# Performance work log

Measured on AMD Instinct MI355X. Metric: run time of the kernel, lower is better.

## Reference

```python
import jax, jax.numpy as jnp
import numpy as np

B, L, D, H, E = 8, 256, 128, 6, 32

def setup_inputs() -> dict:
    key = jax.random.key(0)
    ks = jax.random.split(key, 9)
    s = 0.02
    return {
        "x": jax.random.normal(ks[0], (B, L, D), jnp.float32),
        "weight_adj": jax.random.uniform(ks[1], (B, H, L, L), jnp.float32),
        "e": jax.random.normal(ks[2], (B, L, L, E), jnp.float32),
        "W_w": jax.random.normal(ks[3], (D, D), jnp.float32) * s,
        "W_b": jax.random.normal(ks[4], (D,), jnp.float32) * s,
        "Wx_w": jax.random.normal(ks[5], (H, H + 2 * D + E), jnp.float32) * s,
        "Wx_b": jax.random.normal(ks[6], (H,), jnp.float32) * s,
        "Wxx_w": jax.random.normal(ks[7], (D, D), jnp.float32) * s,
        "Wxx_b": jax.random.normal(ks[8], (D,), jnp.float32) * s,
    }

def reference(x, weight_adj, e, W_w, W_b, Wx_w, Wx_b, Wxx_w, Wxx_b):
    d = x.shape[-1]
    h = weight_adj.shape[1]
    # mean over heads, then graph conv + linear + relu
    adj_avg = weight_adj.mean(axis=1)                      # [B,L,L]
    gcn = jax.nn.relu(jnp.einsum('bij,bjd->bid', adj_avg, x) @ W_w.T + W_b)  # [B,L,d]
    # Wx applied to cat([weight_adj_perm, node_i, node_j, e], -1), decomposed
    # column-wise so the huge [B,L,L,2d+H+E] concat is never materialized;
    # math is identical to Linear(cat(...)).
    Wa  = Wx_w[:, :h]                 # [H,H]
    Wn1 = Wx_w[:, h:h + d]            # [H,d]
    Wn2 = Wx_w[:, h + d:h + 2 * d]    # [H,d]
    We  = Wx_w[:, h + 2 * d:]         # [H,E]
    adj_term = jnp.einsum('bhij,kh->bijk', weight_adj, Wa)   # [B,L,L,H]
    n1 = gcn @ Wn1.T                                          # [B,L,H] (row node)
    n2 = gcn @ Wn2.T                                          # [B,L,H] (col node)
    e_term = jnp.einsum('bije,ke->bijk', e, We)               # [B,L,L,H]
    new_adj = adj_term + n1[:, :, None, :] + n2[:, None, :, :] + e_term + Wx_b
    new_adj = jnp.transpose(new_adj, (0, 3, 1, 2))            # [B,H,L,L]
    out = gcn @ Wxx_w.T + Wxx_b                               # [B,L,d]
    return out, new_adj
```

## Files before the change

### kernel.cpp

```cpp
#include <hip/hip_runtime.h>

#define Bn 8
#define Ln 256
#define Dn 128
#define Hn 6
#define En 32
#define WXROW (Hn + 2*Dn + En)
#define ROWS 4

__global__ __launch_bounds__(256) void k_gcn(
    const float* __restrict__ x, const float* __restrict__ wadj,
    const float* __restrict__ W_w, const float* __restrict__ W_b,
    const float* __restrict__ Wx_w,
    const float* __restrict__ Wxx_w, const float* __restrict__ Wxx_b,
    float* __restrict__ out, float* __restrict__ n1_ws, float* __restrict__ n2_ws)
{
    __shared__ float adj[ROWS][Ln];
    __shared__ float part[8][ROWS][Dn];
    __shared__ float t_s[ROWS][Dn];
    __shared__ float g_s[ROWS][Dn];

    const int t  = threadIdx.x;
    const int b  = blockIdx.x >> 6;
    const int i0 = (blockIdx.x & 63) * ROWS;

    {
        const int r  = t >> 6;
        const int j4 = t & 63;
        const float4* w4 = (const float4*)wadj;
        float4 sum = {0.f, 0.f, 0.f, 0.f};
        #pragma unroll
        for (int h = 0; h < Hn; ++h) {
            const float4 v = w4[(((size_t)b * Hn + h) * Ln + (i0 + r)) * (Ln / 4) + j4];
            sum.x += v.x; sum.y += v.y; sum.z += v.z; sum.w += v.w;
        }
        const float inv_h = 1.0f / 6.0f;
        sum.x *= inv_h; sum.y *= inv_h; sum.z *= inv_h; sum.w *= inv_h;
        ((float4*)&adj[0][0])[r * (Ln / 4) + j4] = sum;
    }
    __syncthreads();

    {
        const int q  = t >> 5;
        const int d4 = t & 31;
        float4 acc[ROWS];
        #pragma unroll
        for (int r = 0; r < ROWS; ++r) acc[r] = {0.f, 0.f, 0.f, 0.f};

        const float4* xp4 = (const float4*)(x + (size_t)b * Ln * Dn) + d4;
        const float4* adj4 = (const float4*)&adj[0][0];
        const int j0 = q * 32;

        #pragma unroll 2
        for (int jj4 = 0; jj4 < 8; ++jj4) {
            const int j = j0 + jj4 * 4;
            const float4 xv0 = xp4[(size_t)(j + 0) * 32];
            const float4 xv1 = xp4[(size_t)(j + 1) * 32];
            const float4 xv2 = xp4[(size_t)(j + 2) * 32];
            const float4 xv3 = xp4[(size_t)(j + 3) * 32];
            #pragma unroll
            for (int r = 0; r < ROWS; ++r) {
                const float4 a = adj4[r * (Ln / 4) + (j >> 2)];
                float4 v = acc[r];
                v.x = fmaf(a.x, xv0.x, v.x); v.y = fmaf(a.x, xv0.y, v.y);
                v.z = fmaf(a.x, xv0.z, v.z); v.w = fmaf(a.x, xv0.w, v.w);
                v.x = fmaf(a.y, xv1.x, v.x); v.y = fmaf(a.y, xv1.y, v.y);
                v.z = fmaf(a.y, xv1.z, v.z); v.w = fmaf(a.y, xv1.w, v.w);
                v.x = fmaf(a.z, xv2.x, v.x); v.y = fmaf(a.z, xv2.y, v.y);
                v.z = fmaf(a.z, xv2.z, v.z); v.w = fmaf(a.z, xv2.w, v.w);
                v.x = fmaf(a.w, xv3.x, v.x); v.y = fmaf(a.w, xv3.y, v.y);
                v.z = fmaf(a.w, xv3.z, v.z); v.w = fmaf(a.w, xv3.w, v.w);
                acc[r] = v;
            }
        }
        #pragma unroll
        for (int r = 0; r < ROWS; ++r)
            ((float4*)&part[q][r][0])[d4] = acc[r];
    }
    __syncthreads();

    {
        const int d  = t & 127;
        const int rr = t >> 7;
        #pragma unroll
        for (int rq = 0; rq < 2; ++rq) {
            const int r = rr + rq * 2;
            float s = 0.f;
            #pragma unroll
            for (int q = 0; q < 8; ++q) s += part[q][r][d];
            t_s[r][d] = s;
        }
    }
    __syncthreads();

    {
        const int s = t >> 7, d = t & 127;
        const int r0 = s, r1 = s + 2;
        float a0 = W_b[d], a1 = a0;
        const float4* wr = (const float4*)(W_w + (size_t)d * Dn);
        const float4* t0 = (const float4*)&t_s[r0][0];
        const float4* t1 = (const float4*)&t_s[r1][0];
        #pragma unroll 8
        for (int c4 = 0; c4 < Dn / 4; ++c4) {
            const float4 w = wr[c4];
            const float4 u0 = t0[c4];
            const float4 u1 = t1[c4];
            a0 = fmaf(u0.x, w.x, a0); a0 = fmaf(u0.y, w.y, a0);
            a0 = fmaf(u0.z, w.z, a0); a0 = fmaf(u0.w, w.w, a0);
            a1 = fmaf(u1.x, w.x, a1); a1 = fmaf(u1.y, w.y, a1);
            a1 = fmaf(u1.z, w.z, a1); a1 = fmaf(u1.w, w.w, a1);
        }
        g_s[r0][d] = fmaxf(a0, 0.f);
        g_s[r1][d] = fmaxf(a1, 0.f);
    }
    __syncthreads();

    {
        const int s = t >> 7, d = t & 127;
        const int r0 = s, r1 = s + 2;
        float a0 = Wxx_b[d], a1 = a0;
        const float4* wr = (const float4*)(Wxx_w + (size_t)d * Dn);
        const float4* g0 = (const float4*)&g_s[r0][0];
        const float4* g1 = (const float4*)&g_s[r1][0];
        #pragma unroll 8
        for (int c4 = 0; c4 < Dn / 4; ++c4) {
            const float4 w = wr[c4];
            const float4 u0 = g0[c4];
            const float4 u1 = g1[c4];
            a0 = fmaf(u0.x, w.x, a0); a0 = fmaf(u0.y, w.y, a0);
            a0 = fmaf(u0.z, w.z, a0); a0 = fmaf(u0.w, w.w, a0);
            a1 = fmaf(u1.x, w.x, a1); a1 = fmaf(u1.y, w.y, a1);
            a1 = fmaf(u1.z, w.z, a1); a1 = fmaf(u1.w, w.w, a1);
        }
        out[((size_t)b * Ln + (i0 + r0)) * Dn + d] = a0;
        out[((size_t)b * Ln + (i0 + r1)) * Dn + d] = a1;
    }

    if (t < ROWS * 2 * Hn) {
        const int r  = t / (2 * Hn);
        const int kk = t % (2 * Hn);
        const int k  = (kk < Hn) ? kk : (kk - Hn);
        const bool isn2 = (kk >= Hn);
        const float* wrow = Wx_w + (size_t)k * WXROW + Hn + (isn2 ? Dn : 0);
        float acc = 0.f;
        #pragma unroll 8
        for (int c = 0; c < Dn; ++c)
            acc = fmaf(g_s[r][c], wrow[c], acc);
        const size_t idx = ((size_t)b * Hn + k) * Ln + (i0 + r);
        if (isn2) n2_ws[idx] = acc;
        else      n1_ws[idx] = acc;
    }
}

#define EPAD 33
__global__ __launch_bounds__(256) void k_adj(
    const float* __restrict__ wadj, const float* __restrict__ e,
    const float* __restrict__ Wx_w, const float* __restrict__ Wx_b,
    const float* __restrict__ n1_ws, const float* __restrict__ n2_ws,
    float* __restrict__ new_adj)
{
    __shared__ float e_lds[Ln * EPAD];
    __shared__ float Wa_s[Hn][Hn];
    __shared__ float We_s[Hn][En];
    __shared__ float bias_n1[Hn];

    const int t = threadIdx.x;
    const int b = blockIdx.x >> 8;
    const int i = blockIdx.x & 255;

    if (t < Hn * Hn) {
        const int k = t / Hn, h = t % Hn;
        Wa_s[k][h] = Wx_w[(size_t)k * WXROW + h];
    }
    if (t >= 64 && t < 64 + Hn * En) {
        const int q = t - 64, k = q / En, c = q % En;
        We_s[k][c] = Wx_w[(size_t)k * WXROW + Hn + 2 * Dn + c];
    }
    if (t >= 32 && t < 32 + Hn) {
        const int k = t - 32;
        bias_n1[k] = Wx_b[k] + n1_ws[((size_t)b * Hn + k) * Ln + i];
    }

    {
        const float4* ep4 = (const float4*)(e + (((size_t)b * Ln + i) * Ln) * En);
        #pragma unroll
        for (int k = 0; k < 8; ++k) {
            const int idx = t + k * 256;
            const float4 v = ep4[idx];
            const int j = idx >> 3;
            const int c = (idx & 7) * 4;
            float* dst = &e_lds[j * EPAD + c];
            dst[0] = v.x; dst[1] = v.y; dst[2] = v.z; dst[3] = v.w;
        }
    }
    __syncthreads();

    const int j = t;

    float ev[En];
    {
        const float* src = &e_lds[j * EPAD];
        #pragma unroll
        for (int c = 0; c < En; ++c) ev[c] = src[c];
    }

    float wv[Hn];
    #pragma unroll
    for (int h = 0; h < Hn; ++h)
        wv[h] = wadj[(((size_t)b * Hn + h) * Ln + i) * Ln + j];

    float n2v[Hn];
    #pragma unroll
    for (int k = 0; k < Hn; ++k)
        n2v[k] = n2_ws[((size_t)b * Hn + k) * Ln + j];

    #pragma unroll
    for (int k = 0; k < Hn; ++k) {
        float acc = bias_n1[k] + n2v[k];
        #pragma unroll
        for (int h = 0; h < Hn; ++h)
            acc = fmaf(wv[h], Wa_s[k][h], acc);
        #pragma unroll
        for (int c = 0; c < En; ++c)
            acc = fmaf(ev[c], We_s[k][c], acc);
        new_adj[(((size_t)b * Hn + k) * Ln + i) * Ln + j] = acc;
    }
}

extern "C" void kernel_launch(void* const* d_in, const int* in_sizes, int n_in,
                              void* d_out, int out_size, void* d_ws, size_t ws_size,
                              hipStream_t stream) {
    const float* x      = (const float*)d_in[0];
    const float* wadj   = (const float*)d_in[1];
    const float* e      = (const float*)d_in[2];
    const float* W_w    = (const float*)d_in[3];
    const float* W_b    = (const float*)d_in[4];
    const float* Wx_w   = (const float*)d_in[5];
    const float* Wx_b   = (const float*)d_in[6];
    const float* Wxx_w  = (const float*)d_in[7];
    const float* Wxx_b  = (const float*)d_in[8];

    float* out      = (float*)d_out;
    float* new_adj  = out + (size_t)Bn * Ln * Dn;

    float* n1_ws = (float*)d_ws;
    float* n2_ws = n1_ws + (size_t)Bn * Hn * Ln;

    k_gcn<<<Bn * (Ln / ROWS), 256, 0, stream>>>(x, wadj, W_w, W_b, Wx_w,
                                                Wxx_w, Wxx_b, out, n1_ws, n2_ws);
    k_adj<<<Bn * Ln, 256, 0, stream>>>(wadj, e, Wx_w, Wx_b, n1_ws, n2_ws, new_adj);
}
```

Before: 146.0 us.

## Split head-averaging kernel, widen GCN blocks, chunk edge-feature staging in adj kernel

The head-mean of weight_adj moves into its own kernel that writes to workspace. The GCN kernel now uses 512 threads and splits the neighbour sum and both 128x128 linears across thread groups, with reductions through shared memory. The adj kernel stages the edge features for 128 columns at a time, which halves its LDS footprint to raise occupancy, and each thread half computes 3 of the 6 output heads. The costs are an extra launch, an avg buffer in workspace, and redundant weight_adj loads across the two thread halves.

```diff
diff --git a/kernel.cpp b/kernel.cpp
--- a/kernel.cpp
+++ b/kernel.cpp
@@ -8,15 +8,34 @@
 #define WXROW (Hn + 2*Dn + En)
 #define ROWS 4
 
-__global__ __launch_bounds__(256) void k_gcn(
-    const float* __restrict__ x, const float* __restrict__ wadj,
+__global__ __launch_bounds__(256) void k_avg(
+    const float* __restrict__ wadj, float* __restrict__ avg)
+{
+    const int g = blockIdx.x * 256 + threadIdx.x;
+    const int j4 = g & 63;
+    const int i  = (g >> 6) & 255;
+    const int b  = g >> 14;
+    const float4* w4 = (const float4*)wadj;
+    float4 s = {0.f, 0.f, 0.f, 0.f};
+    #pragma unroll
+    for (int h = 0; h < Hn; ++h) {
+        const float4 v = w4[(((size_t)b * Hn + h) * Ln + i) * (Ln / 4) + j4];
+        s.x += v.x; s.y += v.y; s.z += v.z; s.w += v.w;
+    }
+    const float inv_h = 1.0f / 6.0f;
+    s.x *= inv_h; s.y *= inv_h; s.z *= inv_h; s.w *= inv_h;
+    ((float4*)avg)[g] = s;
+}
+
+__global__ __launch_bounds__(512) void k_gcn2(
+    const float* __restrict__ x, const float* __restrict__ avg,
     const float* __restrict__ W_w, const float* __restrict__ W_b,
     const float* __restrict__ Wx_w,
     const float* __restrict__ Wxx_w, const float* __restrict__ Wxx_b,
     float* __restrict__ out, float* __restrict__ n1_ws, float* __restrict__ n2_ws)
 {
     __shared__ float adj[ROWS][Ln];
-    __shared__ float part[8][ROWS][Dn];
+    __shared__ float part[16][ROWS][Dn];
     __shared__ float t_s[ROWS][Dn];
     __shared__ float g_s[ROWS][Dn];
 
@@ -24,20 +43,8 @@
     const int b  = blockIdx.x >> 6;
     const int i0 = (blockIdx.x & 63) * ROWS;
 
-    {
-        const int r  = t >> 6;
-        const int j4 = t & 63;
-        const float4* w4 = (const float4*)wadj;
-        float4 sum = {0.f, 0.f, 0.f, 0.f};
-        #pragma unroll
-        for (int h = 0; h < Hn; ++h) {
-            const float4 v = w4[(((size_t)b * Hn + h) * Ln + (i0 + r)) * (Ln / 4) + j4];
-            sum.x += v.x; sum.y += v.y; sum.z += v.z; sum.w += v.w;
-        }
-        const float inv_h = 1.0f / 6.0f;
-        sum.x *= inv_h; sum.y *= inv_h; sum.z *= inv_h; sum.w *= inv_h;
-        ((float4*)&adj[0][0])[r * (Ln / 4) + j4] = sum;
-    }
+    if (t < 256)
+        ((float4*)&adj[0][0])[t] = ((const float4*)avg)[((size_t)b << 14) + (i0 << 6) + t];
     __syncthreads();
 
     {
@@ -46,21 +53,18 @@
         float4 acc[ROWS];
         #pragma unroll
         for (int r = 0; r < ROWS; ++r) acc[r] = {0.f, 0.f, 0.f, 0.f};
-
-        const float4* xp4 = (const float4*)(x + (size_t)b * Ln * Dn) + d4;
+        const float4* xp4  = (const float4*)(x + (size_t)b * Ln * Dn) + d4;
         const float4* adj4 = (const float4*)&adj[0][0];
-        const int j0 = q * 32;
-
-        #pragma unroll 2
-        for (int jj4 = 0; jj4 < 8; ++jj4) {
-            const int j = j0 + jj4 * 4;
+        #pragma unroll
+        for (int jj4 = 0; jj4 < 4; ++jj4) {
+            const int j = q * 16 + jj4 * 4;
             const float4 xv0 = xp4[(size_t)(j + 0) * 32];
             const float4 xv1 = xp4[(size_t)(j + 1) * 32];
             const float4 xv2 = xp4[(size_t)(j + 2) * 32];
             const float4 xv3 = xp4[(size_t)(j + 3) * 32];
             #pragma unroll
             for (int r = 0; r < ROWS; ++r) {
-                const float4 a = adj4[r * (Ln / 4) + (j >> 2)];
+                const float4 a = adj4[r * 64 + (j >> 2)];
                 float4 v = acc[r];
                 v.x = fmaf(a.x, xv0.x, v.x); v.y = fmaf(a.x, xv0.y, v.y);
                 v.z = fmaf(a.x, xv0.z, v.z); v.w = fmaf(a.x, xv0.w, v.w);
@@ -80,60 +84,70 @@
     __syncthreads();
 
     {
-        const int d  = t & 127;
-        const int rr = t >> 7;
-        #pragma unroll
-        for (int rq = 0; rq < 2; ++rq) {
-            const int r = rr + rq * 2;
-            float s = 0.f;
-            #pragma unroll
-            for (int q = 0; q < 8; ++q) s += part[q][r][d];
-            t_s[r][d] = s;
-        }
-    }
-    __syncthreads();
-
-    {
-        const int s = t >> 7, d = t & 127;
-        const int r0 = s, r1 = s + 2;
-        float a0 = W_b[d], a1 = a0;
-        const float4* wr = (const float4*)(W_w + (size_t)d * Dn);
-        const float4* t0 = (const float4*)&t_s[r0][0];
-        const float4* t1 = (const float4*)&t_s[r1][0];
-        #pragma unroll 8
-        for (int c4 = 0; c4 < Dn / 4; ++c4) {
+        const int rr = t >> 7, d = t & 127;
+        float s = 0.f;
+        #pragma unroll
+        for (int q = 0; q < 16; ++q) s += part[q][rr][d];
+        t_s[rr][d] = s;
+    }
+    __syncthreads();
+
+    {
+        const int s = t >> 7, d = t & 127, c0 = s * 32;
+        const float4* wr = (const float4*)(W_w + (size_t)d * Dn + c0);
+        float acc[ROWS] = {0.f, 0.f, 0.f, 0.f};
+        #pragma unroll
+        for (int c4 = 0; c4 < 8; ++c4) {
             const float4 w = wr[c4];
-            const float4 u0 = t0[c4];
-            const float4 u1 = t1[c4];
-            a0 = fmaf(u0.x, w.x, a0); a0 = fmaf(u0.y, w.y, a0);
-            a0 = fmaf(u0.z, w.z, a0); a0 = fmaf(u0.w, w.w, a0);
-            a1 = fmaf(u1.x, w.x, a1); a1 = fmaf(u1.y, w.y, a1);
-            a1 = fmaf(u1.z, w.z, a1); a1 = fmaf(u1.w, w.w, a1);
-        }
-        g_s[r0][d] = fmaxf(a0, 0.f);
-        g_s[r1][d] = fmaxf(a1, 0.f);
-    }
-    __syncthreads();
-
-    {
-        const int s = t >> 7, d = t & 127;
-        const int r0 = s, r1 = s + 2;
-        float a0 = Wxx_b[d], a1 = a0;
-        const float4* wr = (const float4*)(Wxx_w + (size_t)d * Dn);
-        const float4* g0 = (const float4*)&g_s[r0][0];
-        const float4* g1 = (const float4*)&g_s[r1][0];
-        #pragma unroll 8
-        for (int c4 = 0; c4 < Dn / 4; ++c4) {
+            #pragma unroll
+            for (int r = 0; r < ROWS; ++r) {
+                const float4 u = ((const float4*)&t_s[r][c0])[c4];
+                float a = acc[r];
+                a = fmaf(u.x, w.x, a); a = fmaf(u.y, w.y, a);
+                a = fmaf(u.z, w.z, a); a = fmaf(u.w, w.w, a);
+                acc[r] = a;
+            }
+        }
+        #pragma unroll
+        for (int r = 0; r < ROWS; ++r) part[s][r][d] = acc[r];
+    }
+    __syncthreads();
+
+    {
+        const int rr = t >> 7, d = t & 127;
+        const float v = part[0][rr][d] + part[1][rr][d] + part[2][rr][d]
+                      + part[3][rr][d] + W_b[d];
+        g_s[rr][d] = fmaxf(v, 0.f);
+    }
+    __syncthreads();
+
+    {
+        const int s = t >> 7, d = t & 127, c0 = s * 32;
+        const float4* wr = (const float4*)(Wxx_w + (size_t)d * Dn + c0);
+        float acc[ROWS] = {0.f, 0.f, 0.f, 0.f};
+        #pragma unroll
+        for (int c4 = 0; c4 < 8; ++c4) {
             const float4 w = wr[c4];
-            const float4 u0 = g0[c4];
-            const float4 u1 = g1[c4];
-            a0 = fmaf(u0.x, w.x, a0); a0 = fmaf(u0.y, w.y, a0);
-            a0 = fmaf(u0.z, w.z, a0); a0 = fmaf(u0.w, w.w, a0);
-            a1 = fmaf(u1.x, w.x, a1); a1 = fmaf(u1.y, w.y, a1);
-            a1 = fmaf(u1.z, w.z, a1); a1 = fmaf(u1.w, w.w, a1);
-        }
-        out[((size_t)b * Ln + (i0 + r0)) * Dn + d] = a0;
-        out[((size_t)b * Ln + (i0 + r1)) * Dn + d] = a1;
+            #pragma unroll
+            for (int r = 0; r < ROWS; ++r) {
+                const float4 u = ((const float4*)&g_s[r][c0])[c4];
+                float a = acc[r];
+                a = fmaf(u.x, w.x, a); a = fmaf(u.y, w.y, a);
+                a = fmaf(u.z, w.z, a); a = fmaf(u.w, w.w, a);
+                acc[r] = a;
+            }
+        }
+        __syncthreads();
+        #pragma unroll
+        for (int r = 0; r < ROWS; ++r) part[s][r][t & 127] = acc[r];
+    }
+    __syncthreads();
+
+    {
+        const int rr = t >> 7, d = t & 127;
+        const float v = part[0][rr][d] + part[1][rr][d] + part[2][rr][d]
+                      + part[3][rr][d] + Wxx_b[d];
+        out[((size_t)b * Ln + (i0 + rr)) * Dn + d] = v;
     }
 
     if (t < ROWS * 2 * Hn) {
@@ -159,7 +173,7 @@
     const float* __restrict__ n1_ws, const float* __restrict__ n2_ws,
     float* __restrict__ new_adj)
 {
-    __shared__ float e_lds[Ln * EPAD];
+    __shared__ float e_lds[128 * EPAD];
     __shared__ float Wa_s[Hn][Hn];
     __shared__ float We_s[Hn][En];
     __shared__ float bias_n1[Hn];
@@ -181,49 +195,45 @@
         bias_n1[k] = Wx_b[k] + n1_ws[((size_t)b * Hn + k) * Ln + i];
     }
 
-    {
-        const float4* ep4 = (const float4*)(e + (((size_t)b * Ln + i) * Ln) * En);
-        #pragma unroll
-        for (int k = 0; k < 8; ++k) {
-            const int idx = t + k * 256;
-            const float4 v = ep4[idx];
+    const float4* ep4 = (const float4*)(e + (((size_t)b * Ln + i) * Ln) * En);
+    const int s  = t >> 7;
+    const int jl = t & 127;
+
+    #pragma unroll
+    for (int cH = 0; cH < 2; ++cH) {
+        __syncthreads();
+        #pragma unroll
+        for (int p = 0; p < 4; ++p) {
+            const int idx = t + p * 256;
+            const float4 v = ep4[cH * 1024 + idx];
             const int j = idx >> 3;
             const int c = (idx & 7) * 4;
             float* dst = &e_lds[j * EPAD + c];
             dst[0] = v.x; dst[1] = v.y; dst[2] = v.z; dst[3] = v.w;
         }
-    }
-    __syncthreads();
-
-    const int j = t;
-
-    float ev[En];
-    {
-        const float* src = &e_lds[j * EPAD];
-        #pragma unroll
-        for (int c = 0; c < En; ++c) ev[c] = src[c];
-    }
-
-    float wv[Hn];
-    #pragma unroll
-    for (int h = 0; h < Hn; ++h)
-        wv[h] = wadj[(((size_t)b * Hn + h) * Ln + i) * Ln + j];
-
-    float n2v[Hn];
-    #pragma unroll
-    for (int k = 0; k < Hn; ++k)
-        n2v[k] = n2_ws[((size_t)b * Hn + k) * Ln + j];
-
-    #pragma unroll
-    for (int k = 0; k < Hn; ++k) {
-        float acc = bias_n1[k] + n2v[k];
+        __syncthreads();
+
+        const int j = cH * 128 + jl;
+
+        float wv[Hn];
         #pragma unroll
         for (int h = 0; h < Hn; ++h)
-            acc = fmaf(wv[h], Wa_s[k][h], acc);
-        #pragma unroll
-        for (int c = 0; c < En; ++c)
-            acc = fmaf(ev[c], We_s[k][c], acc);
-        new_adj[(((size_t)b * Hn + k) * Ln + i) * Ln + j] = acc;
+            wv[h] = wadj[(((size_t)b * Hn + h) * Ln + i) * Ln + j];
+
+        const float* ev = &e_lds[jl * EPAD];
+
+        #pragma unroll
+        for (int kq = 0; kq < 3; ++kq) {
+            const int k = s * 3 + kq;
+            float acc = bias_n1[k] + n2_ws[((size_t)b * Hn + k) * Ln + j];
+            #pragma unroll
+            for (int h = 0; h < Hn; ++h)
+                acc = fmaf(wv[h], Wa_s[k][h], acc);
+            #pragma unroll
+            for (int c = 0; c < En; ++c)
+                acc = fmaf(ev[c], We_s[k][c], acc);
+            new_adj[(((size_t)b * Hn + k) * Ln + i) * Ln + j] = acc;
+        }
     }
 }
 
@@ -245,8 +255,10 @@
 
     float* n1_ws = (float*)d_ws;
     float* n2_ws = n1_ws + (size_t)Bn * Hn * Ln;
-
-    k_gcn<<<Bn * (Ln / ROWS), 256, 0, stream>>>(x, wadj, W_w, W_b, Wx_w,
-                                                Wxx_w, Wxx_b, out, n1_ws, n2_ws);
+    float* avg   = n2_ws + (size_t)Bn * Hn * Ln;
+
+    k_avg<<<(Bn * Ln * Ln / 4) / 256, 256, 0, stream>>>(wadj, avg);
+    k_gcn2<<<Bn * (Ln / ROWS), 512, 0, stream>>>(x, avg, W_w, W_b, Wx_w,
+                                                 Wxx_w, Wxx_b, out, n1_ws, n2_ws);
     k_adj<<<Bn * Ln, 256, 0, stream>>>(wadj, e, Wx_w, Wx_b, n1_ws, n2_ws, new_adj);
 }
```

New measurement: 150.0 us. 1.03x slower.

## Split adjacency-times-x into tiled split-K kernel with LDS-staged x

Applied to the files above, without the earlier changes.

The head-mean adjacency product with x moves out of the fused gcn kernel into its own kernel. That kernel tiles 32 rows by 64 columns, stages x in shared memory so it is reused across 32 rows, and writes four split-K partials to workspace. A second kernel sums the partials and runs the two linear layers and the n1/n2 projections as before. The aim is to stop every 4-row block from rereading the whole of x from global memory. The cost is an extra launch plus a workspace write and read of four full partial tensors.

```diff
diff --git a/kernel.cpp b/kernel.cpp
--- a/kernel.cpp
+++ b/kernel.cpp
@@ -6,90 +6,96 @@
 #define Hn 6
 #define En 32
 #define WXROW (Hn + 2*Dn + En)
-#define ROWS 4
-
-__global__ __launch_bounds__(256) void k_gcn(
-    const float* __restrict__ x, const float* __restrict__ wadj,
+
+__global__ __launch_bounds__(512) void kT(
+    const float* __restrict__ wadj, const float* __restrict__ x,
+    float* __restrict__ T)
+{
+    __shared__ float adj_s[32][68];
+    __shared__ float x_s[32][128];
+
+    const int t   = threadIdx.x;
+    const int blk = blockIdx.x;
+    const int jq  = blk & 3;
+    const int it  = (blk >> 2) & 7;
+    const int b   = blk >> 5;
+    const int i0  = it * 32;
+
+    {
+        const int row = t >> 4, j4 = t & 15;
+        const float4* w4 = (const float4*)wadj;
+        float4 s = {0.f, 0.f, 0.f, 0.f};
+        #pragma unroll
+        for (int h = 0; h < Hn; ++h) {
+            const float4 v = w4[(((size_t)b * Hn + h) * Ln + i0 + row) * 64 + jq * 16 + j4];
+            s.x += v.x; s.y += v.y; s.z += v.z; s.w += v.w;
+        }
+        const float inv_h = 1.0f / 6.0f;
+        s.x *= inv_h; s.y *= inv_h; s.z *= inv_h; s.w *= inv_h;
+        *(float4*)&adj_s[row][j4 * 4] = s;
+    }
+    __syncthreads();
+
+    const int i  = t & 31;
+    const int dg = t >> 5;
+    float acc[8] = {0.f, 0.f, 0.f, 0.f, 0.f, 0.f, 0.f, 0.f};
+
+    #pragma unroll
+    for (int ch = 0; ch < 2; ++ch) {
+        #pragma unroll
+        for (int rep = 0; rep < 2; ++rep) {
+            const int idx = t + rep * 512;
+            const int jj = idx >> 5, d4 = idx & 31;
+            ((float4*)&x_s[jj][0])[d4] =
+                ((const float4*)(x + ((size_t)b * Ln + jq * 64 + ch * 32 + jj) * Dn))[d4];
+        }
+        __syncthreads();
+        #pragma unroll 4
+        for (int jj = 0; jj < 32; ++jj) {
+            const float a = adj_s[i][ch * 32 + jj];
+            const float4 xv0 = *(const float4*)&x_s[jj][dg * 8];
+            const float4 xv1 = *(const float4*)&x_s[jj][dg * 8 + 4];
+            acc[0] = fmaf(a, xv0.x, acc[0]);
+            acc[1] = fmaf(a, xv0.y, acc[1]);
+            acc[2] = fmaf(a, xv0.z, acc[2]);
+            acc[3] = fmaf(a, xv0.w, acc[3]);
+            acc[4] = fmaf(a, xv1.x, acc[4]);
+            acc[5] = fmaf(a, xv1.y, acc[5]);
+            acc[6] = fmaf(a, xv1.z, acc[6]);
+            acc[7] = fmaf(a, xv1.w, acc[7]);
+        }
+        __syncthreads();
+    }
+
+    float* Tq = T + (size_t)jq * (Bn * Ln * Dn);
+    float4 s0 = {acc[0], acc[1], acc[2], acc[3]};
+    float4 s1 = {acc[4], acc[5], acc[6], acc[7]};
+    float* dst = &Tq[((size_t)b * Ln + i0 + i) * Dn + dg * 8];
+    *(float4*)dst = s0;
+    *(float4*)(dst + 4) = s1;
+}
+
+__global__ __launch_bounds__(256) void kG(
+    const float* __restrict__ T,
     const float* __restrict__ W_w, const float* __restrict__ W_b,
     const float* __restrict__ Wx_w,
     const float* __restrict__ Wxx_w, const float* __restrict__ Wxx_b,
     float* __restrict__ out, float* __restrict__ n1_ws, float* __restrict__ n2_ws)
 {
-    __shared__ float adj[ROWS][Ln];
-    __shared__ float part[8][ROWS][Dn];
-    __shared__ float t_s[ROWS][Dn];
-    __shared__ float g_s[ROWS][Dn];
+    __shared__ float t_s[4][Dn];
+    __shared__ float g_s[4][Dn];
 
     const int t  = threadIdx.x;
     const int b  = blockIdx.x >> 6;
-    const int i0 = (blockIdx.x & 63) * ROWS;
-
-    {
-        const int r  = t >> 6;
-        const int j4 = t & 63;
-        const float4* w4 = (const float4*)wadj;
-        float4 sum = {0.f, 0.f, 0.f, 0.f};
-        #pragma unroll
-        for (int h = 0; h < Hn; ++h) {
-            const float4 v = w4[(((size_t)b * Hn + h) * Ln + (i0 + r)) * (Ln / 4) + j4];
-            sum.x += v.x; sum.y += v.y; sum.z += v.z; sum.w += v.w;
-        }
-        const float inv_h = 1.0f / 6.0f;
-        sum.x *= inv_h; sum.y *= inv_h; sum.z *= inv_h; sum.w *= inv_h;
-        ((float4*)&adj[0][0])[r * (Ln / 4) + j4] = sum;
-    }
-    __syncthreads();
-
-    {
-        const int q  = t >> 5;
-        const int d4 = t & 31;
-        float4 acc[ROWS];
-        #pragma unroll
-        for (int r = 0; r < ROWS; ++r) acc[r] = {0.f, 0.f, 0.f, 0.f};
-
-        const float4* xp4 = (const float4*)(x + (size_t)b * Ln * Dn) + d4;
-        const float4* adj4 = (const float4*)&adj[0][0];
-        const int j0 = q * 32;
-
-        #pragma unroll 2
-        for (int jj4 = 0; jj4 < 8; ++jj4) {
-            const int j = j0 + jj4 * 4;
-            const float4 xv0 = xp4[(size_t)(j + 0) * 32];
-            const float4 xv1 = xp4[(size_t)(j + 1) * 32];
-            const float4 xv2 = xp4[(size_t)(j + 2) * 32];
-            const float4 xv3 = xp4[(size_t)(j + 3) * 32];
-            #pragma unroll
-            for (int r = 0; r < ROWS; ++r) {
-                const float4 a = adj4[r * (Ln / 4) + (j >> 2)];
-                float4 v = acc[r];
-                v.x = fmaf(a.x, xv0.x, v.x); v.y = fmaf(a.x, xv0.y, v.y);
-                v.z = fmaf(a.x, xv0.z, v.z); v.w = fmaf(a.x, xv0.w, v.w);
-                v.x = fmaf(a.y, xv1.x, v.x); v.y = fmaf(a.y, xv1.y, v.y);
-                v.z = fmaf(a.y, xv1.z, v.z); v.w = fmaf(a.y, xv1.w, v.w);
-                v.x = fmaf(a.z, xv2.x, v.x); v.y = fmaf(a.z, xv2.y, v.y);
-                v.z = fmaf(a.z, xv2.z, v.z); v.w = fmaf(a.z, xv2.w, v.w);
-                v.x = fmaf(a.w, xv3.x, v.x); v.y = fmaf(a.w, xv3.y, v.y);
-                v.z = fmaf(a.w, xv3.z, v.z); v.w = fmaf(a.w, xv3.w, v.w);
-                acc[r] = v;
-            }
-        }
-        #pragma unroll
-        for (int r = 0; r < ROWS; ++r)
-            ((float4*)&part[q][r][0])[d4] = acc[r];
-    }
-    __syncthreads();
-
-    {
-        const int d  = t & 127;
-        const int rr = t >> 7;
-        #pragma unroll
-        for (int rq = 0; rq < 2; ++rq) {
-            const int r = rr + rq * 2;
-            float s = 0.f;
-            #pragma unroll
-            for (int q = 0; q < 8; ++q) s += part[q][r][d];
-            t_s[r][d] = s;
-        }
+    const int i0 = (blockIdx.x & 63) * 4;
+    const size_t NT = (size_t)Bn * Ln * Dn;
+
+    #pragma unroll
+    for (int rep = 0; rep < 2; ++rep) {
+        const int idx = t + rep * 256;
+        const int r = idx >> 7, d = idx & 127;
+        const size_t g = ((size_t)b * Ln + i0 + r) * Dn + d;
+        t_s[r][d] = T[g] + T[NT + g] + T[2 * NT + g] + T[3 * NT + g];
     }
     __syncthreads();
 
@@ -136,7 +142,7 @@
         out[((size_t)b * Ln + (i0 + r1)) * Dn + d] = a1;
     }
 
-    if (t < ROWS * 2 * Hn) {
+    if (t < 4 * 2 * Hn) {
         const int r  = t / (2 * Hn);
         const int kk = t % (2 * Hn);
         const int k  = (kk < Hn) ? kk : (kk - Hn);
@@ -245,8 +251,10 @@
 
     float* n1_ws = (float*)d_ws;
     float* n2_ws = n1_ws + (size_t)Bn * Hn * Ln;
-
-    k_gcn<<<Bn * (Ln / ROWS), 256, 0, stream>>>(x, wadj, W_w, W_b, Wx_w,
-                                                Wxx_w, Wxx_b, out, n1_ws, n2_ws);
+    float* T     = n2_ws + (size_t)Bn * Hn * Ln;
+
+    kT<<<256, 512, 0, stream>>>(wadj, x, T);
+    kG<<<512, 256, 0, stream>>>(T, W_w, W_b, Wx_w, Wxx_w, Wxx_b,
+                                out, n1_ws, n2_ws);
     k_adj<<<Bn * Ln, 256, 0, stream>>>(wadj, e, Wx_w, Wx_b, n1_ws, n2_ws, new_adj);
 }
```

Result: slower. 151.2 us (+3.6%).

## Prefetch e and weight tiles into registers; halve LDS footprint in k_adj

Applied to the files above, without the earlier changes.

k_adj now issues all eight e loads into registers at kernel start and stages them into a half-size LDS buffer in two phases. Each thread handles 3 of the 6 heads for two column halves instead of all 6 heads for one column. k_gcn prefetches the first x rows and the first W_w/Wxx_w chunks into registers before barriers so global latency overlaps the reductions. The halved LDS footprint may allow more blocks per CU, at the cost of extra barriers, duplicated wadj loads across the two head groups, and higher register pressure.

```diff
diff --git a/kernel.cpp b/kernel.cpp
--- a/kernel.cpp
+++ b/kernel.cpp
@@ -24,43 +24,54 @@
     const int b  = blockIdx.x >> 6;
     const int i0 = (blockIdx.x & 63) * ROWS;
 
+    const int q  = t >> 5;
+    const int d4 = t & 31;
+    const float4* xp4 = (const float4*)(x + (size_t)b * Ln * Dn) + d4;
+    const int j0 = q * 32;
+
+    float4 xpre[8];
+    #pragma unroll
+    for (int p = 0; p < 8; ++p)
+        xpre[p] = xp4[(size_t)(j0 + p) * 32];
+
     {
         const int r  = t >> 6;
         const int j4 = t & 63;
         const float4* w4 = (const float4*)wadj;
-        float4 sum = {0.f, 0.f, 0.f, 0.f};
+        float4 s = {0.f, 0.f, 0.f, 0.f};
         #pragma unroll
         for (int h = 0; h < Hn; ++h) {
-            const float4 v = w4[(((size_t)b * Hn + h) * Ln + (i0 + r)) * (Ln / 4) + j4];
-            sum.x += v.x; sum.y += v.y; sum.z += v.z; sum.w += v.w;
+            const float4 v = w4[(((size_t)b * Hn + h) * Ln + (i0 + r)) * 64 + j4];
+            s.x += v.x; s.y += v.y; s.z += v.z; s.w += v.w;
         }
         const float inv_h = 1.0f / 6.0f;
-        sum.x *= inv_h; sum.y *= inv_h; sum.z *= inv_h; sum.w *= inv_h;
-        ((float4*)&adj[0][0])[r * (Ln / 4) + j4] = sum;
-    }
-    __syncthreads();
-
-    {
-        const int q  = t >> 5;
-        const int d4 = t & 31;
+        s.x *= inv_h; s.y *= inv_h; s.z *= inv_h; s.w *= inv_h;
+        ((float4*)&adj[0][0])[r * 64 + j4] = s;
+    }
+    __syncthreads();
+
+    {
         float4 acc[ROWS];
         #pragma unroll
         for (int r = 0; r < ROWS; ++r) acc[r] = {0.f, 0.f, 0.f, 0.f};
-
-        const float4* xp4 = (const float4*)(x + (size_t)b * Ln * Dn) + d4;
         const float4* adj4 = (const float4*)&adj[0][0];
-        const int j0 = q * 32;
-
-        #pragma unroll 2
-        for (int jj4 = 0; jj4 < 8; ++jj4) {
-            const int j = j0 + jj4 * 4;
-            const float4 xv0 = xp4[(size_t)(j + 0) * 32];
-            const float4 xv1 = xp4[(size_t)(j + 1) * 32];
-            const float4 xv2 = xp4[(size_t)(j + 2) * 32];
-            const float4 xv3 = xp4[(size_t)(j + 3) * 32];
+
+        #pragma unroll
+        for (int blk4 = 0; blk4 < 8; ++blk4) {
+            const int j = j0 + blk4 * 4;
+            float4 xv0, xv1, xv2, xv3;
+            if (blk4 < 2) {
+                xv0 = xpre[blk4 * 4 + 0]; xv1 = xpre[blk4 * 4 + 1];
+                xv2 = xpre[blk4 * 4 + 2]; xv3 = xpre[blk4 * 4 + 3];
+            } else {
+                xv0 = xp4[(size_t)(j + 0) * 32];
+                xv1 = xp4[(size_t)(j + 1) * 32];
+                xv2 = xp4[(size_t)(j + 2) * 32];
+                xv3 = xp4[(size_t)(j + 3) * 32];
+            }
             #pragma unroll
             for (int r = 0; r < ROWS; ++r) {
-                const float4 a = adj4[r * (Ln / 4) + (j >> 2)];
+                const float4 a = adj4[r * 64 + (j >> 2)];
                 float4 v = acc[r];
                 v.x = fmaf(a.x, xv0.x, v.x); v.y = fmaf(a.x, xv0.y, v.y);
                 v.z = fmaf(a.x, xv0.z, v.z); v.w = fmaf(a.x, xv0.w, v.w);
@@ -79,30 +90,37 @@
     }
     __syncthreads();
 
-    {
-        const int d  = t & 127;
-        const int rr = t >> 7;
+    const int dd = t & 127;
+    const int ss = t >> 7;
+
+    float4 wpre[8];
+    {
+        const float4* wr = (const float4*)(W_w + (size_t)dd * Dn);
+        #pragma unroll
+        for (int p = 0; p < 8; ++p) wpre[p] = wr[p];
+    }
+
+    {
         #pragma unroll
         for (int rq = 0; rq < 2; ++rq) {
-            const int r = rr + rq * 2;
+            const int r = ss + rq * 2;
             float s = 0.f;
             #pragma unroll
-            for (int q = 0; q < 8; ++q) s += part[q][r][d];
-            t_s[r][d] = s;
-        }
-    }
-    __syncthreads();
-
-    {
-        const int s = t >> 7, d = t & 127;
-        const int r0 = s, r1 = s + 2;
-        float a0 = W_b[d], a1 = a0;
-        const float4* wr = (const float4*)(W_w + (size_t)d * Dn);
+            for (int qq = 0; qq < 8; ++qq) s += part[qq][r][dd];
+            t_s[r][dd] = s;
+        }
+    }
+    __syncthreads();
+
+    {
+        const int r0 = ss, r1 = ss + 2;
+        float a0 = W_b[dd], a1 = a0;
+        const float4* wr = (const float4*)(W_w + (size_t)dd * Dn);
         const float4* t0 = (const float4*)&t_s[r0][0];
         const float4* t1 = (const float4*)&t_s[r1][0];
-        #pragma unroll 8
+        #pragma unroll
         for (int c4 = 0; c4 < Dn / 4; ++c4) {
-            const float4 w = wr[c4];
+            const float4 w = (c4 < 8) ? wpre[c4] : wr[c4];
             const float4 u0 = t0[c4];
             const float4 u1 = t1[c4];
             a0 = fmaf(u0.x, w.x, a0); a0 = fmaf(u0.y, w.y, a0);
@@ -110,21 +128,25 @@
             a1 = fmaf(u1.x, w.x, a1); a1 = fmaf(u1.y, w.y, a1);
             a1 = fmaf(u1.z, w.z, a1); a1 = fmaf(u1.w, w.w, a1);
         }
-        g_s[r0][d] = fmaxf(a0, 0.f);
-        g_s[r1][d] = fmaxf(a1, 0.f);
-    }
-    __syncthreads();
-
-    {
-        const int s = t >> 7, d = t & 127;
-        const int r0 = s, r1 = s + 2;
-        float a0 = Wxx_b[d], a1 = a0;
-        const float4* wr = (const float4*)(Wxx_w + (size_t)d * Dn);
+        g_s[r0][dd] = fmaxf(a0, 0.f);
+        g_s[r1][dd] = fmaxf(a1, 0.f);
+    }
+    {
+        const float4* wr = (const float4*)(Wxx_w + (size_t)dd * Dn);
+        #pragma unroll
+        for (int p = 0; p < 8; ++p) wpre[p] = wr[p];
+    }
+    __syncthreads();
+
+    {
+        const int r0 = ss, r1 = ss + 2;
+        float a0 = Wxx_b[dd], a1 = a0;
+        const float4* wr = (const float4*)(Wxx_w + (size_t)dd * Dn);
         const float4* g0 = (const float4*)&g_s[r0][0];
         const float4* g1 = (const float4*)&g_s[r1][0];
-        #pragma unroll 8
+        #pragma unroll
         for (int c4 = 0; c4 < Dn / 4; ++c4) {
-            const float4 w = wr[c4];
+            const float4 w = (c4 < 8) ? wpre[c4] : wr[c4];
             const float4 u0 = g0[c4];
             const float4 u1 = g1[c4];
             a0 = fmaf(u0.x, w.x, a0); a0 = fmaf(u0.y, w.y, a0);
@@ -132,8 +154,8 @@
             a1 = fmaf(u1.x, w.x, a1); a1 = fmaf(u1.y, w.y, a1);
             a1 = fmaf(u1.z, w.z, a1); a1 = fmaf(u1.w, w.w, a1);
         }
-        out[((size_t)b * Ln + (i0 + r0)) * Dn + d] = a0;
-        out[((size_t)b * Ln + (i0 + r1)) * Dn + d] = a1;
+        out[((size_t)b * Ln + (i0 + r0)) * Dn + dd] = a0;
+        out[((size_t)b * Ln + (i0 + r1)) * Dn + dd] = a1;
     }
 
     if (t < ROWS * 2 * Hn) {
@@ -159,7 +181,7 @@
     const float* __restrict__ n1_ws, const float* __restrict__ n2_ws,
     float* __restrict__ new_adj)
 {
-    __shared__ float e_lds[Ln * EPAD];
+    __shared__ float e_lds[128 * EPAD];
     __shared__ float Wa_s[Hn][Hn];
     __shared__ float We_s[Hn][En];
     __shared__ float bias_n1[Hn];
@@ -168,6 +190,14 @@
     const int b = blockIdx.x >> 8;
     const int i = blockIdx.x & 255;
 
+    const float4* ep4 = (const float4*)(e + (((size_t)b * Ln + i) * Ln) * En);
+
+    float4 A[4], Bv[4];
+    #pragma unroll
+    for (int p = 0; p < 4; ++p) A[p]  = ep4[t + p * 256];
+    #pragma unroll
+    for (int p = 0; p < 4; ++p) Bv[p] = ep4[1024 + t + p * 256];
+
     if (t < Hn * Hn) {
         const int k = t / Hn, h = t % Hn;
         Wa_s[k][h] = Wx_w[(size_t)k * WXROW + h];
@@ -181,49 +211,64 @@
         bias_n1[k] = Wx_b[k] + n1_ws[((size_t)b * Hn + k) * Ln + i];
     }
 
-    {
-        const float4* ep4 = (const float4*)(e + (((size_t)b * Ln + i) * Ln) * En);
-        #pragma unroll
-        for (int k = 0; k < 8; ++k) {
-            const int idx = t + k * 256;
-            const float4 v = ep4[idx];
-            const int j = idx >> 3;
-            const int c = (idx & 7) * 4;
-            float* dst = &e_lds[j * EPAD + c];
-            dst[0] = v.x; dst[1] = v.y; dst[2] = v.z; dst[3] = v.w;
-        }
-    }
-    __syncthreads();
-
-    const int j = t;
-
-    float ev[En];
-    {
-        const float* src = &e_lds[j * EPAD];
-        #pragma unroll
-        for (int c = 0; c < En; ++c) ev[c] = src[c];
-    }
-
-    float wv[Hn];
-    #pragma unroll
-    for (int h = 0; h < Hn; ++h)
-        wv[h] = wadj[(((size_t)b * Hn + h) * Ln + i) * Ln + j];
-
-    float n2v[Hn];
-    #pragma unroll
-    for (int k = 0; k < Hn; ++k)
-        n2v[k] = n2_ws[((size_t)b * Hn + k) * Ln + j];
-
-    #pragma unroll
-    for (int k = 0; k < Hn; ++k) {
-        float acc = bias_n1[k] + n2v[k];
+    #pragma unroll
+    for (int p = 0; p < 4; ++p) {
+        const int idx = t + p * 256;
+        const int j = idx >> 3;
+        const int c = (idx & 7) * 4;
+        float* dst = &e_lds[j * EPAD + c];
+        dst[0] = A[p].x; dst[1] = A[p].y; dst[2] = A[p].z; dst[3] = A[p].w;
+    }
+    __syncthreads();
+
+    const int s  = t >> 7;
+    const int jl = t & 127;
+
+    #pragma unroll
+    for (int cH = 0; cH < 2; ++cH) {
+        const int j = cH * 128 + jl;
+
+        float wv[Hn];
         #pragma unroll
         for (int h = 0; h < Hn; ++h)
-            acc = fmaf(wv[h], Wa_s[k][h], acc);
-        #pragma unroll
-        for (int c = 0; c < En; ++c)
-            acc = fmaf(ev[c], We_s[k][c], acc);
-        new_adj[(((size_t)b * Hn + k) * Ln + i) * Ln + j] = acc;
+            wv[h] = wadj[(((size_t)b * Hn + h) * Ln + i) * Ln + j];
+
+        float n2v[3];
+        #pragma unroll
+        for (int kq = 0; kq < 3; ++kq)
+            n2v[kq] = n2_ws[((size_t)b * Hn + s * 3 + kq) * Ln + j];
+
+        const float* ev = &e_lds[jl * EPAD];
+        float evr[En];
+        #pragma unroll
+        for (int c = 0; c < En; ++c) evr[c] = ev[c];
+
+        #pragma unroll
+        for (int kq = 0; kq < 3; ++kq) {
+            const int k = s * 3 + kq;
+            float acc = bias_n1[k] + n2v[kq];
+            #pragma unroll
+            for (int h = 0; h < Hn; ++h)
+                acc = fmaf(wv[h], Wa_s[k][h], acc);
+            #pragma unroll
+            for (int c = 0; c < En; ++c)
+                acc = fmaf(evr[c], We_s[k][c], acc);
+            new_adj[(((size_t)b * Hn + k) * Ln + i) * Ln + j] = acc;
+        }
+
+        if (cH == 0) {
+            __syncthreads();
+            #pragma unroll
+            for (int p = 0; p < 4; ++p) {
+                const int idx = t + p * 256;
+                const int jj = idx >> 3;
+                const int c = (idx & 7) * 4;
+                float* dst = &e_lds[jj * EPAD + c];
+                dst[0] = Bv[p].x; dst[1] = Bv[p].y;
+                dst[2] = Bv[p].z; dst[3] = Bv[p].w;
+            }
+            __syncthreads();
+        }
     }
 }
 
```

After: 147.4 us. No clear change (+1.0%).
